# Kernel tuning notes

Measured on AMD Instinct MI355X. Metric: run time of the kernel, lower is better.

Reference implementation:

```python
import jax
import jax.numpy as jnp
from jax import lax
import numpy as np

V, E, H, H2, C, B, L = 50000, 256, 256, 128, 12, 64, 512
START, STOP = 10, 11
IMPOSSIBLE = -10000.0


def setup_inputs() -> dict:
    key = jax.random.key(0)
    ks = jax.random.split(key, 30)
    rn = lambda k, s, sc=0.1: jax.random.normal(k, s, jnp.float32) * sc
    d = {}
    d["sentence"] = jax.random.randint(ks[0], (B, L), 0, V)
    d["masks"] = jnp.ones((B, L), jnp.float32)
    d["emb_table"] = rn(ks[1], (V, E))
    i = 2
    for layer, din in ((1, E), (2, H)):
        for dr in ("f", "r"):
            d["w_ih_%s%d" % (dr, layer)] = rn(ks[i], (4 * H2, din)); i += 1
            d["w_hh_%s%d" % (dr, layer)] = rn(ks[i], (4 * H2, H2)); i += 1
            d["b_ih_%s%d" % (dr, layer)] = rn(ks[i], (4 * H2,)); i += 1
            d["b_hh_%s%d" % (dr, layer)] = rn(ks[i], (4 * H2,)); i += 1
    d["w_out"] = rn(ks[i], (C, H)); i += 1
    d["b_out"] = rn(ks[i], (C,)); i += 1
    tr = jax.random.normal(ks[i], (C, C), jnp.float32); i += 1
    d["transitions"] = tr.at[START, :].set(IMPOSSIBLE).at[:, STOP].set(IMPOSSIBLE)
    for nm in ("h0_1", "c0_1", "h0_2", "c0_2"):
        d[nm] = rn(ks[i], (2, B, H2), 1.0); i += 1
    return d


def _lstm_dir(x, h0, c0, w_ih, w_hh, b_ih, b_hh, reverse):
    # x: [L, B, Din]; PyTorch LSTM gate order: i, f, g, o
    b = b_ih + b_hh
    def step(carry, xt):
        h, c = carry
        g = xt @ w_ih.T + h @ w_hh.T + b  # [B, 4*H2]
        i, f, gg, o = jnp.split(g, 4, axis=-1)
        c = jax.nn.sigmoid(f) * c + jax.nn.sigmoid(i) * jnp.tanh(gg)
        h = jax.nn.sigmoid(o) * jnp.tanh(c)
        return (h, c), h
    _, hs = lax.scan(step, (h0, c0), x, reverse=reverse)
    return hs  # [L, B, H2]


def _bilstm(x, h0, c0, pf, pr):
    hf = _lstm_dir(x, h0[0], c0[0], *pf, reverse=False)
    hr = _lstm_dir(x, h0[1], c0[1], *pr, reverse=True)
    return jnp.concatenate([hf, hr], axis=-1)  # [L, B, H]


def reference(sentence, masks, emb_table,
              w_ih_f1, w_hh_f1, b_ih_f1, b_hh_f1, w_ih_r1, w_hh_r1, b_ih_r1, b_hh_r1,
              w_ih_f2, w_hh_f2, b_ih_f2, b_hh_f2, w_ih_r2, w_hh_r2, b_ih_r2, b_hh_r2,
              w_out, b_out, transitions, h0_1, c0_1, h0_2, c0_2):
    Bb, Ll = sentence.shape
    # faithful to the original: embedding output is .view()'d (reshaped), not transposed
    embeds = emb_table[sentence].reshape(Ll, Bb, -1)  # [L, B, E]
    out1 = _bilstm(embeds, h0_1, c0_1,
                   (w_ih_f1, w_hh_f1, b_ih_f1, b_hh_f1),
                   (w_ih_r1, w_hh_r1, b_ih_r1, b_hh_r1))
    out2 = _bilstm(out1, h0_2, c0_2,
                   (w_ih_f2, w_hh_f2, b_ih_f2, b_hh_f2),
                   (w_ih_r2, w_hh_r2, b_ih_r2, b_hh_r2))
    feats = out2.reshape(Bb, Ll, -1) @ w_out.T + b_out  # [B, L, C]
    Cc = feats.shape[-1]

    # Viterbi forward pass over time
    init = jnp.full((Bb, Cc), IMPOSSIBLE, jnp.float32).at[:, START].set(0.0)
    def vstep(ms, inp):
        emit, m = inp  # [B, C], [B]
        acc = ms[:, None, :] + transitions[None]  # [B, C_to, C_from]
        bp = jnp.argmax(acc, axis=-1)             # [B, C]
        sc = jnp.max(acc, axis=-1) + emit
        mm = m[:, None]
        return sc * mm + ms * (1.0 - mm), bp
    final, bps = lax.scan(vstep, init, (feats.transpose(1, 0, 2), masks.T))  # bps: [L, B, C]
    final = final + transitions[STOP]
    best_score = final.max(axis=-1)        # [B]
    best_tag = jnp.argmax(final, axis=-1)  # [B]

    # vectorized backtrace: tag[len-1] = best_tag; tag[t] = bps[t+1][tag[t+1]]
    lengths = masks.sum(axis=1).astype(jnp.int32)  # [B]
    bps_next = jnp.concatenate([bps[1:], bps[-1:]], axis=0)  # bps_next[t] = bps[t+1]
    ts = jnp.arange(Ll)
    def bstep(cur, inp):
        t, bpn = inp  # bpn: [B, C]
        nxt = jnp.take_along_axis(bpn, cur[:, None], axis=1)[:, 0]
        new = jnp.where(t >= lengths - 1, best_tag, nxt)
        return new, new
    _, path = lax.scan(bstep, best_tag, (ts, bps_next), reverse=True)  # [L, B]
    path = path.T  # [B, L]
    path = jnp.where(ts[None, :] < lengths[:, None], path, 0)
    return best_score, path
```

## Files before the change

kernel.cpp:

```cpp
#include <hip/hip_runtime.h>
#include <math.h>

#define VSZ   50000
#define EDIM  256
#define HDIM  256
#define H2D   128
#define NCLS  12
#define NB    64
#define NL    512
#define G4    512
#define NNC   1024
#define MM    32768
#define START_TAG 10
#define STOP_TAG  11
#define IMPOSSIBLE -10000.0f

__device__ __forceinline__ float sigmoidf_(float x) {
    return 1.0f / (1.0f + expf(-x));
}

template <bool GATHER>
__global__ __launch_bounds__(256)
void gemm_gates(const float* __restrict__ A,
                const int*   __restrict__ gidx,
                const float* __restrict__ wf,
                const float* __restrict__ wr,
                const float* __restrict__ bihf, const float* __restrict__ bhhf,
                const float* __restrict__ bihr, const float* __restrict__ bhhr,
                float* __restrict__ out)
{
    __shared__ __align__(16) float As[32][132];
    __shared__ __align__(16) float Bs[32][132];

    const int tid = threadIdx.x;
    const int n0  = blockIdx.x * 128;
    const int m0  = blockIdx.y * 128;
    const int ty  = tid >> 4;
    const int tx  = tid & 15;

    float acc[8][8];
#pragma unroll
    for (int i = 0; i < 8; ++i)
#pragma unroll
        for (int j = 0; j < 8; ++j) acc[i][j] = 0.0f;

    const bool  fwdside = (n0 < 512);
    const float* wsrc   = fwdside ? wf : wr;
    const int    nbase  = fwdside ? n0 : (n0 - 512);

    int srcA[4];
#pragma unroll
    for (int it = 0; it < 4; ++it) {
        int li  = tid + it * 256;
        int row = m0 + (li >> 3);
        srcA[it] = GATHER ? gidx[row] : row;
    }

    for (int kt = 0; kt < 8; ++kt) {
#pragma unroll
        for (int it = 0; it < 4; ++it) {
            int li = tid + it * 256;
            int r  = li >> 3;
            int c4 = li & 7;
            float4 v = ((const float4*)A)[(size_t)srcA[it] * 64 + kt * 8 + c4];
            As[c4 * 4 + 0][r] = v.x;
            As[c4 * 4 + 1][r] = v.y;
            As[c4 * 4 + 2][r] = v.z;
            As[c4 * 4 + 3][r] = v.w;
        }
#pragma unroll
        for (int it = 0; it < 4; ++it) {
            int li = tid + it * 256;
            int r  = li >> 3;
            int c4 = li & 7;
            float4 v = ((const float4*)wsrc)[(size_t)(nbase + r) * 64 + kt * 8 + c4];
            Bs[c4 * 4 + 0][r] = v.x;
            Bs[c4 * 4 + 1][r] = v.y;
            Bs[c4 * 4 + 2][r] = v.z;
            Bs[c4 * 4 + 3][r] = v.w;
        }
        __syncthreads();

#pragma unroll
        for (int k = 0; k < 32; ++k) {
            float a[8], b[8];
            *(float4*)&a[0] = *(const float4*)&As[k][ty * 8];
            *(float4*)&a[4] = *(const float4*)&As[k][ty * 8 + 4];
            *(float4*)&b[0] = *(const float4*)&Bs[k][tx * 8];
            *(float4*)&b[4] = *(const float4*)&Bs[k][tx * 8 + 4];
#pragma unroll
            for (int i = 0; i < 8; ++i)
#pragma unroll
                for (int j = 0; j < 8; ++j)
                    acc[i][j] = fmaf(a[i], b[j], acc[i][j]);
        }
        __syncthreads();
    }

    float bias[8];
#pragma unroll
    for (int j = 0; j < 8; ++j) {
        int gn = n0 + tx * 8 + j;
        bias[j] = fwdside ? (bihf[gn] + bhhf[gn]) : (bihr[gn - 512] + bhhr[gn - 512]);
    }
#pragma unroll
    for (int i = 0; i < 8; ++i) {
        int m = m0 + ty * 8 + i;
        float4 s0, s1;
        s0.x = acc[i][0] + bias[0]; s0.y = acc[i][1] + bias[1];
        s0.z = acc[i][2] + bias[2]; s0.w = acc[i][3] + bias[3];
        s1.x = acc[i][4] + bias[4]; s1.y = acc[i][5] + bias[5];
        s1.z = acc[i][6] + bias[6]; s1.w = acc[i][7] + bias[7];
        float4* op = (float4*)(out + (size_t)m * NNC + n0 + tx * 8);
        op[0] = s0;
        op[1] = s1;
    }
}

__global__ __launch_bounds__(512, 2)
void lstm_rec(const float* __restrict__ gx,
              const float* __restrict__ whf,
              const float* __restrict__ whr,
              const float* __restrict__ h0,
              const float* __restrict__ c0,
              float* __restrict__ out)
{
    __shared__ __align__(16) float h_lds[H2D];
    __shared__ __align__(16) float gates[G4];

    const int j   = threadIdx.x;
    const int dir = blockIdx.x >> 6;
    const int bb  = blockIdx.x & 63;
    const float* W = dir ? whr : whf;

    float w[H2D];
#pragma unroll
    for (int k4 = 0; k4 < 32; ++k4) {
        float4 v = ((const float4*)W)[(size_t)j * 32 + k4];
        w[4 * k4 + 0] = v.x; w[4 * k4 + 1] = v.y;
        w[4 * k4 + 2] = v.z; w[4 * k4 + 3] = v.w;
    }

    float creg = 0.0f;
    if (j < H2D) {
        h_lds[j] = h0[dir * (NB * H2D) + bb * H2D + j];
        creg     = c0[dir * (NB * H2D) + bb * H2D + j];
    }
    __syncthreads();

    const int chunk = j >> 7;
    const float4* h4 = (const float4*)h_lds;

    for (int ti = 0; ti < NL; ++ti) {
        const int t = dir ? (NL - 1 - ti) : ti;
        const size_t m = (size_t)t * NB + bb;

        const float gxv = gx[m * NNC + dir * 512 + j];

        float dot = 0.0f;
#pragma unroll
        for (int k4 = 0; k4 < 32; ++k4) {
            float4 hv = h4[k4];
            dot = fmaf(w[4 * k4 + 0], hv.x, dot);
            dot = fmaf(w[4 * k4 + 1], hv.y, dot);
            dot = fmaf(w[4 * k4 + 2], hv.z, dot);
            dot = fmaf(w[4 * k4 + 3], hv.w, dot);
        }
        const float pre = dot + gxv;
        const float act = (chunk == 2) ? tanhf(pre) : sigmoidf_(pre);
        gates[j] = act;
        __syncthreads();

        if (j < H2D) {
            const float ig = gates[j];
            const float fg = gates[j + 128];
            const float gg = gates[j + 256];
            const float og = gates[j + 384];
            creg = fg * creg + ig * gg;
            const float hnew = og * tanhf(creg);
            h_lds[j] = hnew;
            out[m * HDIM + dir * H2D + j] = hnew;
        }
        __syncthreads();
    }
}

__global__ __launch_bounds__(256)
void feats_kernel(const float* __restrict__ out2,
                  const float* __restrict__ w_out,
                  const float* __restrict__ b_out,
                  float* __restrict__ feats)
{
    __shared__ __align__(16) float wl[NCLS * HDIM];
    const int tid = threadIdx.x;
#pragma unroll
    for (int i = 0; i < NCLS; ++i) wl[tid + i * 256] = w_out[tid + i * 256];
    __syncthreads();

    const int m = blockIdx.x * 256 + tid;
    float acc[NCLS];
#pragma unroll
    for (int c = 0; c < NCLS; ++c) acc[c] = 0.0f;

    const float4* x4 = (const float4*)out2 + (size_t)m * 64;
    const float4* w4 = (const float4*)wl;
    for (int k4 = 0; k4 < 64; ++k4) {
        float4 x = x4[k4];
#pragma unroll
        for (int c = 0; c < NCLS; ++c) {
            float4 wv = w4[c * 64 + k4];
            acc[c] = fmaf(x.x, wv.x, acc[c]);
            acc[c] = fmaf(x.y, wv.y, acc[c]);
            acc[c] = fmaf(x.z, wv.z, acc[c]);
            acc[c] = fmaf(x.w, wv.w, acc[c]);
        }
    }
#pragma unroll
    for (int c = 0; c < NCLS; ++c)
        feats[(size_t)m * NCLS + c] = acc[c] + b_out[c];
}

__global__ __launch_bounds__(64)
void viterbi_fwd(const float* __restrict__ feats,
                 const float* __restrict__ masks,
                 const float* __restrict__ trans,
                 float* __restrict__ best_score,
                 unsigned char* __restrict__ bps,
                 int* __restrict__ best_tag)
{
    const int b    = blockIdx.x;
    const int lane = threadIdx.x;

    float tr[NCLS];
#pragma unroll
    for (int jj = 0; jj < NCLS; ++jj)
        tr[jj] = (lane < NCLS) ? trans[lane * NCLS + jj] : 0.0f;

    float msv = (lane == START_TAG) ? 0.0f : IMPOSSIBLE;

    for (int t = 0; t < NL; ++t) {
        const float emit = (lane < NCLS) ? feats[((size_t)b * NL + t) * NCLS + lane] : 0.0f;
        const float mt   = masks[b * NL + t];

        float best = -3.4e38f;
        int   bj   = 0;
#pragma unroll
        for (int jj = 0; jj < NCLS; ++jj) {
            float msj = __shfl(msv, jj);
            float v   = msj + tr[jj];
            if (v > best) { best = v; bj = jj; }
        }
        const float sc = best + emit;
        msv = mt * sc + (1.0f - mt) * msv;
        if (lane < NCLS)
            bps[((size_t)t * NB + b) * NCLS + lane] = (unsigned char)bj;
    }

    const float fin = (lane < NCLS) ? (msv + trans[STOP_TAG * NCLS + lane]) : -3.4e38f;
    float bv = -3.4e38f;
    int   bt = 0;
#pragma unroll
    for (int jj = 0; jj < NCLS; ++jj) {
        float v = __shfl(fin, jj);
        if (v > bv) { bv = v; bt = jj; }
    }
    if (lane == 0) {
        best_score[b] = bv;
        best_tag[b]   = bt;
    }
}

__global__ __launch_bounds__(64)
void backtrace(const unsigned char* __restrict__ bps,
               const int* __restrict__ best_tag,
               const float* __restrict__ masks,
               float* __restrict__ path_out)
{
    const int b = threadIdx.x;
    float s = 0.0f;
    for (int t = 0; t < NL; ++t) s += masks[b * NL + t];
    const int len  = (int)(s + 0.5f);
    const int btag = best_tag[b];

    int cur = btag;
    for (int t = NL - 1; t >= 0; --t) {
        const int tb  = (t == NL - 1) ? (NL - 1) : (t + 1);
        const int nxt = bps[((size_t)tb * NB + b) * NCLS + cur];
        const int val = (t >= len - 1) ? btag : nxt;
        cur = val;
        path_out[(size_t)b * NL + t] = (t < len) ? (float)val : 0.0f;
    }
}

extern "C" void kernel_launch(void* const* d_in, const int* in_sizes, int n_in,
                              void* d_out, int out_size, void* d_ws, size_t ws_size,
                              hipStream_t stream)
{
    const int*   sentence = (const int*)  d_in[0];
    const float* masks    = (const float*)d_in[1];
    const float* emb      = (const float*)d_in[2];
    const float* w_ih_f1  = (const float*)d_in[3];
    const float* w_hh_f1  = (const float*)d_in[4];
    const float* b_ih_f1  = (const float*)d_in[5];
    const float* b_hh_f1  = (const float*)d_in[6];
    const float* w_ih_r1  = (const float*)d_in[7];
    const float* w_hh_r1  = (const float*)d_in[8];
    const float* b_ih_r1  = (const float*)d_in[9];
    const float* b_hh_r1  = (const float*)d_in[10];
    const float* w_ih_f2  = (const float*)d_in[11];
    const float* w_hh_f2  = (const float*)d_in[12];
    const float* b_ih_f2  = (const float*)d_in[13];
    const float* b_hh_f2  = (const float*)d_in[14];
    const float* w_ih_r2  = (const float*)d_in[15];
    const float* w_hh_r2  = (const float*)d_in[16];
    const float* b_ih_r2  = (const float*)d_in[17];
    const float* b_hh_r2  = (const float*)d_in[18];
    const float* w_out    = (const float*)d_in[19];
    const float* b_out    = (const float*)d_in[20];
    const float* trans    = (const float*)d_in[21];
    const float* h0_1     = (const float*)d_in[22];
    const float* c0_1     = (const float*)d_in[23];
    const float* h0_2     = (const float*)d_in[24];
    const float* c0_2     = (const float*)d_in[25];

    float* gx    = (float*)d_ws;
    float* out1  = gx   + (size_t)MM * NNC;
    float* out2  = out1 + (size_t)MM * HDIM;
    float* feats = out2 + (size_t)MM * HDIM;
    int*   btag  = (int*)(feats + (size_t)MM * NCLS);
    unsigned char* bps = (unsigned char*)(btag + 64);

    dim3 gemm_grid(NNC / 128, MM / 128);

    gemm_gates<true><<<gemm_grid, 256, 0, stream>>>(
        emb, sentence, w_ih_f1, w_ih_r1, b_ih_f1, b_hh_f1, b_ih_r1, b_hh_r1, gx);
    lstm_rec<<<128, 512, 0, stream>>>(gx, w_hh_f1, w_hh_r1, h0_1, c0_1, out1);

    gemm_gates<false><<<gemm_grid, 256, 0, stream>>>(
        out1, nullptr, w_ih_f2, w_ih_r2, b_ih_f2, b_hh_f2, b_ih_r2, b_hh_r2, gx);
    lstm_rec<<<128, 512, 0, stream>>>(gx, w_hh_f2, w_hh_r2, h0_2, c0_2, out2);

    feats_kernel<<<MM / 256, 256, 0, stream>>>(out2, w_out, b_out, feats);
    viterbi_fwd<<<NB, 64, 0, stream>>>(feats, masks, trans, (float*)d_out, bps, btag);
    backtrace<<<1, 64, 0, stream>>>(bps, btag, masks, (float*)d_out + 64);
}
```

Before: 1.858 ms.

## Fuse Viterbi and backtrace, prefetch gate inputs, remap GEMM threads per wavefront

Several changes land together. The Viterbi forward pass and the backtrace are fused into one kernel that keeps backpointers and the path in LDS, which removes a launch and the global round trip through the backpointer buffer. The LSTM recurrence prefetches the next timestep's input-gate value during the barrier, splits the dot product into four independent accumulators, and pins the weights in registers. The GEMM thread-to-tile mapping is changed to a per-wavefront 2x2 layout to alter the LDS access pattern; the four-way split also changes floating-point summation order slightly.

```diff
diff --git a/kernel.cpp b/kernel.cpp
--- a/kernel.cpp
+++ b/kernel.cpp
@@ -35,18 +35,25 @@
     const int tid = threadIdx.x;
     const int n0  = blockIdx.x * 128;
     const int m0  = blockIdx.y * 128;
-    const int ty  = tid >> 4;
-    const int tx  = tid & 15;
+
+    const int w    = tid >> 6;
+    const int lane = tid & 63;
+    const int wm   = w >> 1;
+    const int wn   = w & 1;
+    const int am   = lane >> 3;
+    const int bn   = lane & 7;
+    const int ma   = wm * 64 + am * 8;
+    const int nb   = wn * 64 + bn * 8;
 
     float acc[8][8];
 #pragma unroll
     for (int i = 0; i < 8; ++i)
 #pragma unroll
-        for (int j = 0; j < 8; ++j) acc[i][j] = 0.0f;
-
-    const bool  fwdside = (n0 < 512);
-    const float* wsrc   = fwdside ? wf : wr;
-    const int    nbase  = fwdside ? n0 : (n0 - 512);
+        for (int jj = 0; jj < 8; ++jj) acc[i][jj] = 0.0f;
+
+    const bool   fwdside = (n0 < 512);
+    const float* wsrc    = fwdside ? wf : wr;
+    const int    nbase   = fwdside ? n0 : (n0 - 512);
 
     int srcA[4];
 #pragma unroll
@@ -84,34 +91,34 @@
 #pragma unroll
         for (int k = 0; k < 32; ++k) {
             float a[8], b[8];
-            *(float4*)&a[0] = *(const float4*)&As[k][ty * 8];
-            *(float4*)&a[4] = *(const float4*)&As[k][ty * 8 + 4];
-            *(float4*)&b[0] = *(const float4*)&Bs[k][tx * 8];
-            *(float4*)&b[4] = *(const float4*)&Bs[k][tx * 8 + 4];
+            *(float4*)&a[0] = *(const float4*)&As[k][ma];
+            *(float4*)&a[4] = *(const float4*)&As[k][ma + 4];
+            *(float4*)&b[0] = *(const float4*)&Bs[k][nb];
+            *(float4*)&b[4] = *(const float4*)&Bs[k][nb + 4];
 #pragma unroll
             for (int i = 0; i < 8; ++i)
 #pragma unroll
-                for (int j = 0; j < 8; ++j)
-                    acc[i][j] = fmaf(a[i], b[j], acc[i][j]);
+                for (int jj = 0; jj < 8; ++jj)
+                    acc[i][jj] = fmaf(a[i], b[jj], acc[i][jj]);
         }
         __syncthreads();
     }
 
     float bias[8];
 #pragma unroll
-    for (int j = 0; j < 8; ++j) {
-        int gn = n0 + tx * 8 + j;
-        bias[j] = fwdside ? (bihf[gn] + bhhf[gn]) : (bihr[gn - 512] + bhhr[gn - 512]);
+    for (int jj = 0; jj < 8; ++jj) {
+        int gn = n0 + nb + jj;
+        bias[jj] = fwdside ? (bihf[gn] + bhhf[gn]) : (bihr[gn - 512] + bhhr[gn - 512]);
     }
 #pragma unroll
     for (int i = 0; i < 8; ++i) {
-        int m = m0 + ty * 8 + i;
+        int m = m0 + ma + i;
         float4 s0, s1;
         s0.x = acc[i][0] + bias[0]; s0.y = acc[i][1] + bias[1];
         s0.z = acc[i][2] + bias[2]; s0.w = acc[i][3] + bias[3];
         s1.x = acc[i][4] + bias[4]; s1.y = acc[i][5] + bias[5];
         s1.z = acc[i][6] + bias[6]; s1.w = acc[i][7] + bias[7];
-        float4* op = (float4*)(out + (size_t)m * NNC + n0 + tx * 8);
+        float4* op = (float4*)(out + (size_t)m * NNC + n0 + nb);
         op[0] = s0;
         op[1] = s1;
     }
@@ -133,13 +140,13 @@
     const int bb  = blockIdx.x & 63;
     const float* W = dir ? whr : whf;
 
-    float w[H2D];
-#pragma unroll
-    for (int k4 = 0; k4 < 32; ++k4) {
-        float4 v = ((const float4*)W)[(size_t)j * 32 + k4];
-        w[4 * k4 + 0] = v.x; w[4 * k4 + 1] = v.y;
-        w[4 * k4 + 2] = v.z; w[4 * k4 + 3] = v.w;
-    }
+    float4 w4[32];
+#pragma unroll
+    for (int k = 0; k < 32; ++k)
+        w4[k] = ((const float4*)W)[(size_t)j * 32 + k];
+#pragma unroll
+    for (int k = 0; k < 32; ++k)
+        asm volatile("" : "+v"(w4[k].x), "+v"(w4[k].y), "+v"(w4[k].z), "+v"(w4[k].w));
 
     float creg = 0.0f;
     if (j < H2D) {
@@ -148,28 +155,35 @@
     }
     __syncthreads();
 
+    const float4* h4 = (const float4*)h_lds;
     const int chunk = j >> 7;
-    const float4* h4 = (const float4*)h_lds;
+    const size_t gx_off = (size_t)dir * 512 + j;
+
+    const int tfirst = dir ? (NL - 1) : 0;
+    float gx_cur = gx[((size_t)tfirst * NB + bb) * NNC + gx_off];
 
     for (int ti = 0; ti < NL; ++ti) {
         const int t = dir ? (NL - 1 - ti) : ti;
         const size_t m = (size_t)t * NB + bb;
 
-        const float gxv = gx[m * NNC + dir * 512 + j];
-
-        float dot = 0.0f;
-#pragma unroll
-        for (int k4 = 0; k4 < 32; ++k4) {
-            float4 hv = h4[k4];
-            dot = fmaf(w[4 * k4 + 0], hv.x, dot);
-            dot = fmaf(w[4 * k4 + 1], hv.y, dot);
-            dot = fmaf(w[4 * k4 + 2], hv.z, dot);
-            dot = fmaf(w[4 * k4 + 3], hv.w, dot);
-        }
-        const float pre = dot + gxv;
+        float d0 = 0.f, d1 = 0.f, d2 = 0.f, d3 = 0.f;
+#pragma unroll
+        for (int k = 0; k < 32; ++k) {
+            const float4 hv = h4[k];
+            d0 = fmaf(w4[k].x, hv.x, d0);
+            d1 = fmaf(w4[k].y, hv.y, d1);
+            d2 = fmaf(w4[k].z, hv.z, d2);
+            d3 = fmaf(w4[k].w, hv.w, d3);
+        }
+        const float pre = ((d0 + d1) + (d2 + d3)) + gx_cur;
         const float act = (chunk == 2) ? tanhf(pre) : sigmoidf_(pre);
         gates[j] = act;
         __syncthreads();
+
+        if (ti + 1 < NL) {
+            const int tn = dir ? (NL - 2 - ti) : (ti + 1);
+            gx_cur = gx[((size_t)tn * NB + bb) * NNC + gx_off];
+        }
 
         if (j < H2D) {
             const float ig = gates[j];
@@ -221,13 +235,14 @@
 }
 
 __global__ __launch_bounds__(64)
-void viterbi_fwd(const float* __restrict__ feats,
+void viterbi_crf(const float* __restrict__ feats,
                  const float* __restrict__ masks,
                  const float* __restrict__ trans,
-                 float* __restrict__ best_score,
-                 unsigned char* __restrict__ bps,
-                 int* __restrict__ best_tag)
-{
+                 float* __restrict__ out)
+{
+    __shared__ unsigned char bpl[NL][NCLS];
+    __shared__ float pathl[NL];
+
     const int b    = blockIdx.x;
     const int lane = threadIdx.x;
 
@@ -237,10 +252,19 @@
         tr[jj] = (lane < NCLS) ? trans[lane * NCLS + jj] : 0.0f;
 
     float msv = (lane == START_TAG) ? 0.0f : IMPOSSIBLE;
+    float len = 0.0f;
+
+    float emit_n = (lane < NCLS) ? feats[((size_t)b * NL) * NCLS + lane] : 0.0f;
+    float mt_n   = masks[b * NL];
 
     for (int t = 0; t < NL; ++t) {
-        const float emit = (lane < NCLS) ? feats[((size_t)b * NL + t) * NCLS + lane] : 0.0f;
-        const float mt   = masks[b * NL + t];
+        const float emit = emit_n;
+        const float mt   = mt_n;
+        if (t + 1 < NL) {
+            emit_n = (lane < NCLS) ? feats[((size_t)b * NL + t + 1) * NCLS + lane] : 0.0f;
+            mt_n   = masks[b * NL + t + 1];
+        }
+        len += mt;
 
         float best = -3.4e38f;
         int   bj   = 0;
@@ -253,7 +277,7 @@
         const float sc = best + emit;
         msv = mt * sc + (1.0f - mt) * msv;
         if (lane < NCLS)
-            bps[((size_t)t * NB + b) * NCLS + lane] = (unsigned char)bj;
+            bpl[t][lane] = (unsigned char)bj;
     }
 
     const float fin = (lane < NCLS) ? (msv + trans[STOP_TAG * NCLS + lane]) : -3.4e38f;
@@ -264,32 +288,26 @@
         float v = __shfl(fin, jj);
         if (v > bv) { bv = v; bt = jj; }
     }
-    if (lane == 0) {
-        best_score[b] = bv;
-        best_tag[b]   = bt;
-    }
-}
-
-__global__ __launch_bounds__(64)
-void backtrace(const unsigned char* __restrict__ bps,
-               const int* __restrict__ best_tag,
-               const float* __restrict__ masks,
-               float* __restrict__ path_out)
-{
-    const int b = threadIdx.x;
-    float s = 0.0f;
-    for (int t = 0; t < NL; ++t) s += masks[b * NL + t];
-    const int len  = (int)(s + 0.5f);
-    const int btag = best_tag[b];
-
-    int cur = btag;
+    if (lane == 0) out[b] = bv;
+
+    const int ilen = (int)(len + 0.5f);
+
+    __syncthreads();
+
+    int cur = bt;
     for (int t = NL - 1; t >= 0; --t) {
         const int tb  = (t == NL - 1) ? (NL - 1) : (t + 1);
-        const int nxt = bps[((size_t)tb * NB + b) * NCLS + cur];
-        const int val = (t >= len - 1) ? btag : nxt;
+        const int nxt = bpl[tb][cur];
+        const int val = (t >= ilen - 1) ? bt : nxt;
         cur = val;
-        path_out[(size_t)b * NL + t] = (t < len) ? (float)val : 0.0f;
-    }
+        if (lane == 0) pathl[t] = (t < ilen) ? (float)val : 0.0f;
+    }
+    __syncthreads();
+
+    float* po = out + 64 + (size_t)b * NL;
+#pragma unroll
+    for (int i = 0; i < NL / 64; ++i)
+        po[lane + i * 64] = pathl[lane + i * 64];
 }
 
 extern "C" void kernel_launch(void* const* d_in, const int* in_sizes, int n_in,
@@ -327,8 +345,6 @@
     float* out1  = gx   + (size_t)MM * NNC;
     float* out2  = out1 + (size_t)MM * HDIM;
     float* feats = out2 + (size_t)MM * HDIM;
-    int*   btag  = (int*)(feats + (size_t)MM * NCLS);
-    unsigned char* bps = (unsigned char*)(btag + 64);
 
     dim3 gemm_grid(NNC / 128, MM / 128);
 
@@ -341,6 +357,5 @@
     lstm_rec<<<128, 512, 0, stream>>>(gx, w_hh_f2, w_hh_r2, h0_2, c0_2, out2);
 
     feats_kernel<<<MM / 256, 256, 0, stream>>>(out2, w_out, b_out, feats);
-    viterbi_fwd<<<NB, 64, 0, stream>>>(feats, masks, trans, (float*)d_out, bps, btag);
-    backtrace<<<1, 64, 0, stream>>>(bps, btag, masks, (float*)d_out + 64);
-}
+    viterbi_crf<<<NB, 64, 0, stream>>>(feats, masks, trans, (float*)d_out);
+}
```

After: 1.872 ms. Within noise of the previous version (+0.7%).
